# Kernel optimization log

Measured on AMD Instinct MI355X. Metric: run time of the kernel, lower is better.

Reference implementation:

```python
import jax, jax.numpy as jnp
import numpy as np

B, N, F, P, E, EMB = 32, 51, 4, 137, 408, 32


def _gcn_norm(edge_index, num_nodes):
    # add self loops, symmetric normalization D^-1/2 (A+I) D^-1/2 (PyG gcn_norm)
    loops = jnp.arange(num_nodes, dtype=edge_index.dtype)
    src = jnp.concatenate([edge_index[0], loops])
    dst = jnp.concatenate([edge_index[1], loops])
    w = jnp.ones(src.shape[0], dtype=jnp.float32)
    deg = jnp.zeros((num_nodes,), jnp.float32).at[dst].add(w)
    dinv = jnp.where(deg > 0, 1.0 / jnp.sqrt(deg), 0.0)
    norm = dinv[src] * w * dinv[dst]
    return src, dst, norm


def _gcn_conv(x, W, b, src, dst, norm, num_nodes):
    # x: [B, P, N, Fin] -> [B, P, N, Fout]; linear first, then normalized aggregation
    xw = jnp.einsum('bpnf,fe->bpne', x, W)
    msg = xw[:, :, src, :] * norm[None, None, :, None]
    out = jnp.zeros(xw.shape[:2] + (num_nodes, W.shape[1]), xw.dtype).at[:, :, dst, :].add(msg)
    return out + b


def _forward(x, edge_index, conv_z_w, conv_z_b, conv_r_w, conv_r_b, conv_h_w, conv_h_b,
             lin_z_w, lin_z_b, lin_r_w, lin_r_b, lin_h_w, lin_h_b, attention,
             lin1_w, lin1_b, lin2_w, lin2_b, lin3_w, lin3_b):
    num_nodes = x.shape[1]
    xt = jnp.transpose(x, (0, 3, 1, 2))  # [B, P, N, F] -- periods as a batch dim
    src, dst, norm = _gcn_norm(edge_index, num_nodes)
    # A3TGCN2 never updates H across periods (H stays None -> zeros), so all 137
    # TGCN2 cell evaluations are independent and can be vectorized over P.
    cz = _gcn_conv(xt, conv_z_w, conv_z_b, src, dst, norm, num_nodes)
    ch = _gcn_conv(xt, conv_h_w, conv_h_b, src, dst, norm, num_nodes)
    zeros_h = jnp.zeros_like(cz)
    # Z = sigmoid(lin_z([conv_z(x), H])) with H = 0
    Z = jax.nn.sigmoid(jnp.concatenate([cz, zeros_h], axis=-1) @ lin_z_w + lin_z_b)
    # R gate multiplies H (= 0) so it has no effect on the output; omitted (DCE-equivalent).
    # H_tilde = tanh(lin_h([conv_h(x), H * R])) with H = 0
    Ht = jnp.tanh(jnp.concatenate([ch, zeros_h], axis=-1) @ lin_h_w + lin_h_b)
    Hp = (1.0 - Z) * Ht  # Z*H + (1-Z)*H_tilde with H = 0 -> [B, P, N, EMB]
    probs = jax.nn.softmax(attention)
    h = jnp.einsum('p,bpne->bne', probs, Hp)  # attention-weighted accumulation
    h = jax.nn.relu(h)
    # dropout(0.2) is identity in eval mode
    h = jax.nn.relu(h @ lin1_w + lin1_b)
    h = h @ lin2_w + lin2_b            # [B, N, 1]
    h = h.reshape(-1, num_nodes)       # [B, N]
    h = jax.nn.sigmoid(h @ lin3_w + lin3_b)  # [B, 1]
    return h.reshape(-1)


def setup_inputs() -> dict:
    key = jax.random.key(0)
    ks = jax.random.split(key, 16)
    def rn(k, shape, scale=0.1):
        return jax.random.normal(k, shape, dtype=jnp.float32) * scale
    return {
        'x': jax.random.normal(ks[0], (B, N, F, P), dtype=jnp.float32),
        'edge_index': jax.random.randint(ks[1], (2, E), 0, N, dtype=jnp.int32),
        'conv_z_w': rn(ks[2], (F, EMB)), 'conv_z_b': jnp.zeros((EMB,), jnp.float32),
        'conv_r_w': rn(ks[3], (F, EMB)), 'conv_r_b': jnp.zeros((EMB,), jnp.float32),
        'conv_h_w': rn(ks[4], (F, EMB)), 'conv_h_b': jnp.zeros((EMB,), jnp.float32),
        'lin_z_w': rn(ks[5], (2 * EMB, EMB)), 'lin_z_b': jnp.zeros((EMB,), jnp.float32),
        'lin_r_w': rn(ks[6], (2 * EMB, EMB)), 'lin_r_b': jnp.zeros((EMB,), jnp.float32),
        'lin_h_w': rn(ks[7], (2 * EMB, EMB)), 'lin_h_b': jnp.zeros((EMB,), jnp.float32),
        'attention': jax.random.uniform(ks[8], (P,), dtype=jnp.float32),
        'lin1_w': rn(ks[9], (EMB, 32)), 'lin1_b': jnp.zeros((32,), jnp.float32),
        'lin2_w': rn(ks[10], (32, 1)), 'lin2_b': jnp.zeros((1,), jnp.float32),
        'lin3_w': rn(ks[11], (N, 1)), 'lin3_b': jnp.zeros((1,), jnp.float32),
    }


def reference(x, edge_index, conv_z_w, conv_z_b, conv_r_w, conv_r_b, conv_h_w, conv_h_b,
              lin_z_w, lin_z_b, lin_r_w, lin_r_b, lin_h_w, lin_h_b, attention,
              lin1_w, lin1_b, lin2_w, lin2_b, lin3_w, lin3_b):
    return _forward(x, edge_index, conv_z_w, conv_z_b, conv_r_w, conv_r_b, conv_h_w, conv_h_b,
                    lin_z_w, lin_z_b, lin_r_w, lin_r_b, lin_h_w, lin_h_b, attention,
                    lin1_w, lin1_b, lin2_w, lin2_b, lin3_w, lin3_b)
```

## Files before the change

kernel.cpp:

```cpp
#include <hip/hip_runtime.h>
#include <hip/hip_bf16.h>

#define NND 51
#define FIN 4
#define PDIM 137
#define EMB 32
#define EE 408
#define BD 32
#define PC 5
#define NCH 28
#define NE (NND*EMB)
#define ROWP 52
#define AMP_N (NND*ROWP)

#define WS_AMP   0
#define WS_PROBS 2656
#define WS_WU    2800
#define WS_BEFF  3056
#define WS_H     3120

__global__ __launch_bounds__(256) void precompute_kernel(
    const int* __restrict__ ei, const float* __restrict__ att,
    const float* __restrict__ Wz, const float* __restrict__ bz,
    const float* __restrict__ Wh, const float* __restrict__ bh,
    const float* __restrict__ Uz, const float* __restrict__ bz2,
    const float* __restrict__ Uh, const float* __restrict__ bh2,
    float* __restrict__ ws)
{
    __shared__ float deg[NND], dinv[NND];
    __shared__ float Am[AMP_N];
    __shared__ float Us[2][EMB * EMB];
    __shared__ float Ws2[2][FIN * EMB];
    __shared__ float atts[PDIM];
    __shared__ float inv_sum;
    int t = threadIdx.x;
    for (int i = t; i < AMP_N; i += 256) Am[i] = 0.0f;
    if (t < NND) deg[t] = 0.0f;
    for (int i = t; i < EMB * EMB; i += 256) { Us[0][i] = Uz[i]; Us[1][i] = Uh[i]; }
    if (t < FIN * EMB) { Ws2[0][t] = Wz[t]; Ws2[1][t] = Wh[t]; }
    if (t < PDIM) atts[t] = att[t];
    __syncthreads();
    for (int e = t; e < EE; e += 256) atomicAdd(&deg[ei[EE + e]], 1.0f);
    __syncthreads();
    if (t < NND) dinv[t] = rsqrtf(deg[t] + 1.0f);
    __syncthreads();
    for (int e = t; e < EE; e += 256) {
        int s = ei[e], d = ei[EE + e];
        atomicAdd(&Am[d * ROWP + s], dinv[s] * dinv[d]);
    }
    {
        int g = t >> 7, f = (t >> 5) & 3, e = t & 31;
        float a = 0.0f;
        for (int k = 0; k < EMB; k++) a += Ws2[g][f * EMB + k] * Us[g][k * EMB + e];
        ws[WS_WU + t] = a;
    }
    if (t < 64) {
        int g = t >> 5, e = t & 31;
        const float* bb = g ? bh : bz;
        const float* b2 = g ? bh2 : bz2;
        float a = b2[e];
        for (int k = 0; k < EMB; k++) a += bb[k] * Us[g][k * EMB + e];
        ws[WS_BEFF + t] = a;
    }
    __syncthreads();
    if (t < NND) Am[t * ROWP + t] += dinv[t] * dinv[t];
    if (t == 0) {
        float m = -1e30f;
        for (int p = 0; p < PDIM; p++) m = fmaxf(m, atts[p]);
        float s = 0.0f;
        for (int p = 0; p < PDIM; p++) { float v = __expf(atts[p] - m); atts[p] = v; s += v; }
        inv_sum = 1.0f / s;
    }
    __syncthreads();
    for (int i = t; i < AMP_N; i += 256) ws[WS_AMP + i] = Am[i];
    if (t < PDIM) ws[WS_PROBS + t] = atts[t] * inv_sum;
}

__global__ __launch_bounds__(256) void main_kernel(
    const float* __restrict__ x, const float* __restrict__ ws,
    float* __restrict__ h)
{
    __shared__ __align__(16) float AmP[AMP_N];
    __shared__ __align__(16) float xs5[PC * FIN * ROWP];
    __shared__ __align__(16) float aggA[PC * NND * 4];
    __shared__ float wus[256];
    __shared__ float beffs[64];
    __shared__ float probs5[PC];

    int t = threadIdx.x;
    int b = blockIdx.y;
    int c = blockIdx.x;
    int p0 = c * PC;
    int npp = min(PC, PDIM - p0);

    for (int i = t; i < AMP_N / 4; i += 256)
        ((float4*)AmP)[i] = ((const float4*)(ws + WS_AMP))[i];
    wus[t] = ws[WS_WU + t];
    if (t < 64) beffs[t] = ws[WS_BEFF + t];
    if (t < npp) probs5[t] = ws[WS_PROBS + p0 + t];
    if (t < PC * FIN) xs5[t * ROWP + NND] = 0.0f;
    if (t < NND * FIN) {
        int n = t >> 2, f = t & 3;
        const float* xp = &x[((b * NND + n) * FIN + f) * PDIM + p0];
        for (int pp = 0; pp < npp; pp++) xs5[(pp * FIN + f) * ROWP + n] = xp[pp];
    }
    __syncthreads();

    int e = t & 31, r = t >> 5;
    float wuz[4], wuh[4];
    #pragma unroll
    for (int f = 0; f < 4; f++) { wuz[f] = wus[f * EMB + e]; wuh[f] = wus[128 + f * EMB + e]; }
    float bez = beffs[e], beh = beffs[32 + e];

    #pragma unroll
    for (int j = 0; j < 4; j++) {
        int i = t + 256 * j;
        if (i < npp * 204) {
            int pp = i / 204, rr = i - pp * 204;
            int d = rr >> 2, f = rr & 3;
            const float4* Ar = (const float4*)&AmP[d * ROWP];
            const float4* xr = (const float4*)&xs5[(pp * FIN + f) * ROWP];
            float a = 0.0f;
            #pragma unroll
            for (int s4 = 0; s4 < 13; s4++) {
                float4 A4 = Ar[s4], X4 = xr[s4];
                a += A4.x * X4.x + A4.y * X4.y + A4.z * X4.z + A4.w * X4.w;
            }
            aggA[pp * 204 + rr] = a;
        }
    }
    __syncthreads();

    float hacc[7] = {0, 0, 0, 0, 0, 0, 0};
    for (int pp = 0; pp < npp; pp++) {
        float pr = probs5[pp];
        #pragma unroll
        for (int k = 0; k < 7; k++) {
            int d = r + 8 * k;
            if (d < NND) {
                float4 ag = *(const float4*)&aggA[pp * 204 + d * 4];
                float az = bez + ag.x * wuz[0] + ag.y * wuz[1] + ag.z * wuz[2] + ag.w * wuz[3];
                float ah = beh + ag.x * wuh[0] + ag.y * wuh[1] + ag.z * wuh[2] + ag.w * wuh[3];
                float Z  = 1.0f / (1.0f + __expf(-az));
                float Ht = 2.0f / (1.0f + __expf(-2.0f * ah)) - 1.0f;
                hacc[k] += pr * (1.0f - Z) * Ht;
            }
        }
    }
    float* dst = &h[b * NE];
    #pragma unroll
    for (int k = 0; k < 7; k++) {
        int d = r + 8 * k;
        if (d < NND) atomicAdd(&dst[d * EMB + e], hacc[k]);
    }
}

__global__ __launch_bounds__(256) void head_kernel(
    const float* __restrict__ h, const float* __restrict__ W1,
    const float* __restrict__ b1, const float* __restrict__ w2,
    const float* __restrict__ b2, const float* __restrict__ w3,
    const float* __restrict__ b3, float* __restrict__ out)
{
    __shared__ float hs[NE];
    __shared__ float W1s[EMB * EMB];
    __shared__ float b1s[EMB], w2s[EMB];
    __shared__ float w3s[NND];
    __shared__ float wsum[4];
    int t = threadIdx.x, b = blockIdx.x;
    for (int i = t; i < NE; i += 256) hs[i] = fmaxf(h[b * NE + i], 0.0f);
    for (int i = t; i < EMB * EMB; i += 256) W1s[i] = W1[i];
    if (t < EMB) { b1s[t] = b1[t]; w2s[t] = w2[t]; }
    if (t < NND) w3s[t] = w3[t];
    __syncthreads();
    float acc = 0.0f;
    for (int i = t; i < NE; i += 256) {
        int d = i >> 5, e = i & 31;
        float a = b1s[e];
        const float* hr = &hs[d * EMB];
        #pragma unroll
        for (int k = 0; k < EMB; k++) a += hr[k] * W1s[k * EMB + e];
        a = fmaxf(a, 0.0f);
        acc += w3s[d] * w2s[e] * a;
    }
    #pragma unroll
    for (int off = 32; off > 0; off >>= 1) acc += __shfl_down(acc, off);
    if ((t & 63) == 0) wsum[t >> 6] = acc;
    __syncthreads();
    if (t == 0) {
        float s = wsum[0] + wsum[1] + wsum[2] + wsum[3];
        float s3 = 0.0f;
        for (int d = 0; d < NND; d++) s3 += w3s[d];
        float v = s + b2[0] * s3 + b3[0];
        out[b] = 1.0f / (1.0f + __expf(-v));
    }
}

extern "C" void kernel_launch(void* const* d_in, const int* in_sizes, int n_in,
                              void* d_out, int out_size, void* d_ws, size_t ws_size,
                              hipStream_t stream) {
    const float* x         = (const float*)d_in[0];
    const int*   ei        = (const int*)d_in[1];
    const float* conv_z_w  = (const float*)d_in[2];
    const float* conv_z_b  = (const float*)d_in[3];
    const float* conv_h_w  = (const float*)d_in[6];
    const float* conv_h_b  = (const float*)d_in[7];
    const float* lin_z_w   = (const float*)d_in[8];
    const float* lin_z_b   = (const float*)d_in[9];
    const float* lin_h_w   = (const float*)d_in[12];
    const float* lin_h_b   = (const float*)d_in[13];
    const float* attention = (const float*)d_in[14];
    const float* lin1_w    = (const float*)d_in[15];
    const float* lin1_b    = (const float*)d_in[16];
    const float* lin2_w    = (const float*)d_in[17];
    const float* lin2_b    = (const float*)d_in[18];
    const float* lin3_w    = (const float*)d_in[19];
    const float* lin3_b    = (const float*)d_in[20];

    float* ws = (float*)d_ws;
    float* h  = ws + WS_H;

    hipLaunchKernelGGL(precompute_kernel, dim3(1), dim3(256), 0, stream,
                       ei, attention, conv_z_w, conv_z_b, conv_h_w, conv_h_b,
                       lin_z_w, lin_z_b, lin_h_w, lin_h_b, ws);
    hipLaunchKernelGGL(main_kernel, dim3(NCH, BD), dim3(256), 0, stream,
                       x, ws, h);
    hipLaunchKernelGGL(head_kernel, dim3(BD), dim3(256), 0, stream,
                       h, lin1_w, lin1_b, lin2_w, lin2_b, lin3_w, lin3_b,
                       (float*)d_out);
}
```

Baseline: 133.1 us.

## Fuse head into main kernel via last-block counter and zero h in setup

Result: slower. 136.3 us (+2.4%).

```diff
diff --git a/kernel.cpp b/kernel.cpp
--- a/kernel.cpp
+++ b/kernel.cpp
@@ -10,16 +10,30 @@
 #define PC 5
 #define NCH 28
 #define NE (NND*EMB)
-#define ROWP 52
-#define AMP_N (NND*ROWP)
 
 #define WS_AMP   0
-#define WS_PROBS 2656
-#define WS_WU    2800
-#define WS_BEFF  3056
-#define WS_H     3120
-
-__global__ __launch_bounds__(256) void precompute_kernel(
+#define WS_PROBS 2608
+#define WS_WU    2752
+#define WS_BEFF  3008
+#define WS_CNT   3072
+#define WS_H     3104
+
+#define OFF_AS   0
+#define OFF_XS   2604
+#define OFF_AG   3624
+#define OFF_WU   4644
+#define OFF_BE   4900
+#define OFF_PR   4964
+#define OFF_FLAG 4972
+#define SM_N     4976
+#define H_HS     0
+#define H_W1     1632
+#define H_B1     2656
+#define H_W2     2688
+#define H_W3     2720
+#define H_WS     2772
+
+__global__ __launch_bounds__(256) void setup_kernel(
     const int* __restrict__ ei, const float* __restrict__ att,
     const float* __restrict__ Wz, const float* __restrict__ bz,
     const float* __restrict__ Wh, const float* __restrict__ bh,
@@ -27,14 +41,21 @@
     const float* __restrict__ Uh, const float* __restrict__ bh2,
     float* __restrict__ ws)
 {
+    int t = threadIdx.x, blk = blockIdx.x;
+    if (blk > 0) {
+        float4* dst = (float4*)(ws + WS_CNT);
+        const int n4 = (32 + BD * NE) / 4;
+        float4 z = make_float4(0.f, 0.f, 0.f, 0.f);
+        for (int i = (blk - 1) * 256 + t; i < n4; i += 7 * 256) dst[i] = z;
+        return;
+    }
     __shared__ float deg[NND], dinv[NND];
-    __shared__ float Am[AMP_N];
+    __shared__ float Am[2604];
     __shared__ float Us[2][EMB * EMB];
     __shared__ float Ws2[2][FIN * EMB];
     __shared__ float atts[PDIM];
     __shared__ float inv_sum;
-    int t = threadIdx.x;
-    for (int i = t; i < AMP_N; i += 256) Am[i] = 0.0f;
+    for (int i = t; i < 2604; i += 256) Am[i] = 0.0f;
     if (t < NND) deg[t] = 0.0f;
     for (int i = t; i < EMB * EMB; i += 256) { Us[0][i] = Uz[i]; Us[1][i] = Uh[i]; }
     if (t < FIN * EMB) { Ws2[0][t] = Wz[t]; Ws2[1][t] = Wh[t]; }
@@ -46,7 +67,7 @@
     __syncthreads();
     for (int e = t; e < EE; e += 256) {
         int s = ei[e], d = ei[EE + e];
-        atomicAdd(&Am[d * ROWP + s], dinv[s] * dinv[d]);
+        atomicAdd(&Am[d * NND + s], dinv[s] * dinv[d]);
     }
     {
         int g = t >> 7, f = (t >> 5) & 3, e = t & 31;
@@ -63,7 +84,7 @@
         ws[WS_BEFF + t] = a;
     }
     __syncthreads();
-    if (t < NND) Am[t * ROWP + t] += dinv[t] * dinv[t];
+    if (t < NND) Am[t * 52] += dinv[t] * dinv[t];
     if (t == 0) {
         float m = -1e30f;
         for (int p = 0; p < PDIM; p++) m = fmaxf(m, atts[p]);
@@ -72,73 +93,70 @@
         inv_sum = 1.0f / s;
     }
     __syncthreads();
-    for (int i = t; i < AMP_N; i += 256) ws[WS_AMP + i] = Am[i];
+    for (int i = t; i < 2604; i += 256) ws[WS_AMP + i] = Am[i];
     if (t < PDIM) ws[WS_PROBS + t] = atts[t] * inv_sum;
 }
 
-__global__ __launch_bounds__(256) void main_kernel(
-    const float* __restrict__ x, const float* __restrict__ ws,
-    float* __restrict__ h)
+__global__ __launch_bounds__(256) void fused_kernel(
+    const float* __restrict__ x, float* __restrict__ ws,
+    float* __restrict__ h, const float* __restrict__ W1,
+    const float* __restrict__ b1, const float* __restrict__ w2,
+    const float* __restrict__ b2, const float* __restrict__ w3,
+    const float* __restrict__ b3, float* __restrict__ out)
 {
-    __shared__ __align__(16) float AmP[AMP_N];
-    __shared__ __align__(16) float xs5[PC * FIN * ROWP];
-    __shared__ __align__(16) float aggA[PC * NND * 4];
-    __shared__ float wus[256];
-    __shared__ float beffs[64];
-    __shared__ float probs5[PC];
-
+    __shared__ __align__(16) float sm[SM_N];
     int t = threadIdx.x;
     int b = blockIdx.y;
     int c = blockIdx.x;
     int p0 = c * PC;
     int npp = min(PC, PDIM - p0);
 
-    for (int i = t; i < AMP_N / 4; i += 256)
-        ((float4*)AmP)[i] = ((const float4*)(ws + WS_AMP))[i];
-    wus[t] = ws[WS_WU + t];
-    if (t < 64) beffs[t] = ws[WS_BEFF + t];
-    if (t < npp) probs5[t] = ws[WS_PROBS + p0 + t];
-    if (t < PC * FIN) xs5[t * ROWP + NND] = 0.0f;
+    for (int i = t; i < 651; i += 256)
+        ((float4*)(sm + OFF_AS))[i] = ((const float4*)(ws + WS_AMP))[i];
+    sm[OFF_WU + t] = ws[WS_WU + t];
+    if (t < 64) sm[OFF_BE + t] = ws[WS_BEFF + t];
+    if (t < npp) sm[OFF_PR + t] = ws[WS_PROBS + p0 + t];
     if (t < NND * FIN) {
         int n = t >> 2, f = t & 3;
         const float* xp = &x[((b * NND + n) * FIN + f) * PDIM + p0];
-        for (int pp = 0; pp < npp; pp++) xs5[(pp * FIN + f) * ROWP + n] = xp[pp];
+        for (int pp = 0; pp < npp; pp++) sm[OFF_XS + (pp * NND + n) * 4 + f] = xp[pp];
     }
     __syncthreads();
 
     int e = t & 31, r = t >> 5;
     float wuz[4], wuh[4];
     #pragma unroll
-    for (int f = 0; f < 4; f++) { wuz[f] = wus[f * EMB + e]; wuh[f] = wus[128 + f * EMB + e]; }
-    float bez = beffs[e], beh = beffs[32 + e];
-
-    #pragma unroll
-    for (int j = 0; j < 4; j++) {
-        int i = t + 256 * j;
-        if (i < npp * 204) {
-            int pp = i / 204, rr = i - pp * 204;
-            int d = rr >> 2, f = rr & 3;
-            const float4* Ar = (const float4*)&AmP[d * ROWP];
-            const float4* xr = (const float4*)&xs5[(pp * FIN + f) * ROWP];
-            float a = 0.0f;
-            #pragma unroll
-            for (int s4 = 0; s4 < 13; s4++) {
-                float4 A4 = Ar[s4], X4 = xr[s4];
-                a += A4.x * X4.x + A4.y * X4.y + A4.z * X4.z + A4.w * X4.w;
+    for (int f = 0; f < 4; f++) {
+        wuz[f] = sm[OFF_WU + f * EMB + e];
+        wuh[f] = sm[OFF_WU + 128 + f * EMB + e];
+    }
+    float bez = sm[OFF_BE + e], beh = sm[OFF_BE + 32 + e];
+
+    if (t < NND * PC) {
+        int pp = t / NND, d = t - pp * NND;
+        if (pp < npp) {
+            const float*  Ad = sm + OFF_AS + d * NND;
+            const float4* xr = (const float4*)(sm + OFF_XS) + pp * NND;
+            float4 acc = make_float4(0.f, 0.f, 0.f, 0.f);
+            #pragma unroll 3
+            for (int s = 0; s < NND; s++) {
+                float a = Ad[s]; float4 xv = xr[s];
+                acc.x += a * xv.x; acc.y += a * xv.y;
+                acc.z += a * xv.z; acc.w += a * xv.w;
             }
-            aggA[pp * 204 + rr] = a;
+            ((float4*)(sm + OFF_AG))[pp * NND + d] = acc;
         }
     }
     __syncthreads();
 
     float hacc[7] = {0, 0, 0, 0, 0, 0, 0};
     for (int pp = 0; pp < npp; pp++) {
-        float pr = probs5[pp];
+        float pr = sm[OFF_PR + pp];
         #pragma unroll
         for (int k = 0; k < 7; k++) {
             int d = r + 8 * k;
             if (d < NND) {
-                float4 ag = *(const float4*)&aggA[pp * 204 + d * 4];
+                float4 ag = ((const float4*)(sm + OFF_AG))[pp * NND + d];
                 float az = bez + ag.x * wuz[0] + ag.y * wuz[1] + ag.z * wuz[2] + ag.w * wuz[3];
                 float ah = beh + ag.x * wuh[0] + ag.y * wuh[1] + ag.z * wuh[2] + ag.w * wuh[3];
                 float Z  = 1.0f / (1.0f + __expf(-az));
@@ -153,43 +171,43 @@
         int d = r + 8 * k;
         if (d < NND) atomicAdd(&dst[d * EMB + e], hacc[k]);
     }
-}
-
-__global__ __launch_bounds__(256) void head_kernel(
-    const float* __restrict__ h, const float* __restrict__ W1,
-    const float* __restrict__ b1, const float* __restrict__ w2,
-    const float* __restrict__ b2, const float* __restrict__ w3,
-    const float* __restrict__ b3, float* __restrict__ out)
-{
-    __shared__ float hs[NE];
-    __shared__ float W1s[EMB * EMB];
-    __shared__ float b1s[EMB], w2s[EMB];
-    __shared__ float w3s[NND];
-    __shared__ float wsum[4];
-    int t = threadIdx.x, b = blockIdx.x;
-    for (int i = t; i < NE; i += 256) hs[i] = fmaxf(h[b * NE + i], 0.0f);
-    for (int i = t; i < EMB * EMB; i += 256) W1s[i] = W1[i];
-    if (t < EMB) { b1s[t] = b1[t]; w2s[t] = w2[t]; }
-    if (t < NND) w3s[t] = w3[t];
+
+    __syncthreads();
+    if (t == 0) {
+        __threadfence();
+        int old = atomicAdd((int*)(ws + WS_CNT) + b, 1);
+        *(int*)(sm + OFF_FLAG) = (old == NCH - 1);
+    }
+    __syncthreads();
+    if (!*(int*)(sm + OFF_FLAG)) return;
+
+    for (int i = t; i < NE; i += 256) {
+        float v = __hip_atomic_load(&h[b * NE + i], __ATOMIC_RELAXED,
+                                    __HIP_MEMORY_SCOPE_AGENT);
+        sm[H_HS + i] = fmaxf(v, 0.0f);
+    }
+    for (int i = t; i < EMB * EMB; i += 256) sm[H_W1 + i] = W1[i];
+    if (t < EMB) { sm[H_B1 + t] = b1[t]; sm[H_W2 + t] = w2[t]; }
+    if (t < NND) sm[H_W3 + t] = w3[t];
     __syncthreads();
     float acc = 0.0f;
     for (int i = t; i < NE; i += 256) {
-        int d = i >> 5, e = i & 31;
-        float a = b1s[e];
-        const float* hr = &hs[d * EMB];
+        int d = i >> 5, ee = i & 31;
+        float a = sm[H_B1 + ee];
+        const float* hr = sm + H_HS + d * EMB;
         #pragma unroll
-        for (int k = 0; k < EMB; k++) a += hr[k] * W1s[k * EMB + e];
+        for (int k = 0; k < EMB; k++) a += hr[k] * sm[H_W1 + k * EMB + ee];
         a = fmaxf(a, 0.0f);
-        acc += w3s[d] * w2s[e] * a;
+        acc += sm[H_W3 + d] * sm[H_W2 + ee] * a;
     }
     #pragma unroll
     for (int off = 32; off > 0; off >>= 1) acc += __shfl_down(acc, off);
-    if ((t & 63) == 0) wsum[t >> 6] = acc;
+    if ((t & 63) == 0) sm[H_WS + (t >> 6)] = acc;
     __syncthreads();
     if (t == 0) {
-        float s = wsum[0] + wsum[1] + wsum[2] + wsum[3];
+        float s = sm[H_WS] + sm[H_WS + 1] + sm[H_WS + 2] + sm[H_WS + 3];
         float s3 = 0.0f;
-        for (int d = 0; d < NND; d++) s3 += w3s[d];
+        for (int d = 0; d < NND; d++) s3 += sm[H_W3 + d];
         float v = s + b2[0] * s3 + b3[0];
         out[b] = 1.0f / (1.0f + __expf(-v));
     }
@@ -219,12 +237,10 @@
     float* ws = (float*)d_ws;
     float* h  = ws + WS_H;
 
-    hipLaunchKernelGGL(precompute_kernel, dim3(1), dim3(256), 0, stream,
+    hipLaunchKernelGGL(setup_kernel, dim3(8), dim3(256), 0, stream,
                        ei, attention, conv_z_w, conv_z_b, conv_h_w, conv_h_b,
                        lin_z_w, lin_z_b, lin_h_w, lin_h_b, ws);
-    hipLaunchKernelGGL(main_kernel, dim3(NCH, BD), dim3(256), 0, stream,
-                       x, ws, h);
-    hipLaunchKernelGGL(head_kernel, dim3(BD), dim3(256), 0, stream,
-                       h, lin1_w, lin1_b, lin2_w, lin2_b, lin3_w, lin3_b,
-                       (float*)d_out);
+    hipLaunchKernelGGL(fused_kernel, dim3(NCH, BD), dim3(256), 0, stream,
+                       x, ws, h, lin1_w, lin1_b, lin2_w, lin2_b,
+                       lin3_w, lin3_b, (float*)d_out);
 }
```
